# Optimization experiments

Measured on AMD Instinct MI355X. Metric: run time of the kernel, lower is better.

Reference implementation:

```python
import jax, jax.numpy as jnp
import numpy as np

N_TERMS = 500000
TERM_DIM = 300
N_RELS = 40
REL_DIM = 5
BATCH = 500000


def setup_inputs() -> dict:
    key = jax.random.key(0)
    k1, k2, k3, k4, k5, k6 = jax.random.split(key, 6)
    rels = jax.random.randint(k1, (BATCH,), 0, N_RELS)
    terms_L = jax.random.randint(k2, (BATCH,), 0, N_TERMS)
    terms_R = jax.random.randint(k3, (BATCH,), 0, N_TERMS)
    # learned parameters (nn.Embedding weights + assoc tensor)
    term_table = jax.random.normal(k4, (N_TERMS, TERM_DIM), dtype=jnp.float32) * 0.1
    rel_table = jax.random.normal(k5, (N_RELS, REL_DIM), dtype=jnp.float32) * 0.1
    assoc = jax.random.normal(k6, (REL_DIM, TERM_DIM, TERM_DIM), dtype=jnp.float32) * 0.01
    return {
        "rels": rels,
        "terms_L": terms_L,
        "terms_R": terms_R,
        "term_table": term_table,
        "rel_table": rel_table,
        "assoc": assoc,
    }


def reference(rels, terms_L, terms_R, term_table, rel_table, assoc):
    # Gather embeddings
    r = rel_table[rels]          # [B, 5]
    tL = term_table[terms_L]     # [B, D]
    tR = term_table[terms_R]     # [B, D]
    # Trilinear energy: energy_b = sum_{i,j,k} r[b,i] * assoc[i,j,k] * tL[b,j] * tR[b,k]
    # Contract through the small rank-5 relation axis to avoid the original's
    # [B, D, D] intermediate: tmp is only [B, 5, D].
    tmp = jnp.einsum('bj,rjk->brk', tL, assoc)   # [B, 5, D]
    energy = jnp.einsum('brk,bk,br->b', tmp, tR, r)  # [B]
    return energy
```

## Files before the change

### kernel.cpp

```cpp
#include <hip/hip_runtime.h>
#include <hip/hip_bf16.h>

#define DIMT 300
#define DPAD 320
#define NRELS 40
#define RELD 5
#define TILE_M 64
#define MAX_CHUNKS 8192

typedef __attribute__((ext_vector_type(8))) short bf16x8;
typedef __attribute__((ext_vector_type(4))) float f32x4;

#define DESC_OFF 256
#define SORTED_OFF (DESC_OFF + 3*MAX_CHUNKS)
#define MT_OFF_BYTES(B) ((((size_t)(SORTED_OFF + (B)) * 4) + 255) & ~(size_t)255)

__global__ void k_init(int* cnt) {
    int t = threadIdx.x;
    if (t < 64) cnt[t] = 0;
    if (t < 64) cnt[64 + t] = 0;
    if (t == 0) cnt[128] = 0;
}

__global__ void k_hist(const int* __restrict__ rels, int n, int* cnt) {
    __shared__ int l[NRELS];
    int t = threadIdx.x;
    if (t < NRELS) l[t] = 0;
    __syncthreads();
    int b = blockIdx.x * 256 + t;
    if (b < n) atomicAdd(&l[rels[b]], 1);
    __syncthreads();
    if (t < NRELS && l[t]) atomicAdd(&cnt[t], l[t]);
}

__global__ void k_scan(const int* __restrict__ cnt, int* cursor, int* n_chunks,
                       int* desc_rel, int* desc_start, int* desc_end) {
    __shared__ int offs[NRELS + 1];
    __shared__ int coff[NRELS + 1];
    if (threadIdx.x == 0) {
        int s = 0, c = 0;
        for (int r = 0; r < NRELS; r++) {
            offs[r] = s; s += cnt[r];
            coff[r] = c; c += (cnt[r] + TILE_M - 1) / TILE_M;
        }
        offs[NRELS] = s; coff[NRELS] = c;
        *n_chunks = c;
    }
    __syncthreads();
    if (threadIdx.x < NRELS) cursor[threadIdx.x] = offs[threadIdx.x];
    for (int r = 0; r < NRELS; r++) {
        int nch = (cnt[r] + TILE_M - 1) / TILE_M;
        int cend = offs[r] + cnt[r];
        for (int c = threadIdx.x; c < nch; c += 256) {
            int st = offs[r] + c * TILE_M;
            desc_rel[coff[r] + c] = r;
            desc_start[coff[r] + c] = st;
            desc_end[coff[r] + c] = min(st + TILE_M, cend);
        }
    }
}

__global__ void k_scatter(const int* __restrict__ rels, int n, int* cursor,
                          int* __restrict__ sorted) {
    __shared__ int l[NRELS];
    __shared__ int base[NRELS];
    int t = threadIdx.x;
    if (t < NRELS) l[t] = 0;
    __syncthreads();
    int b = blockIdx.x * 256 + t;
    int r = -1, loc = 0;
    if (b < n) { r = rels[b]; loc = atomicAdd(&l[r], 1); }
    __syncthreads();
    if (t < NRELS && l[t]) base[t] = atomicAdd(&cursor[t], l[t]);
    __syncthreads();
    if (b < n) sorted[base[r] + loc] = b;
}

__global__ void k_build_mt(const float* __restrict__ rel_table,
                           const float* __restrict__ assoc,
                           __hip_bfloat16* __restrict__ Mt) {
    int r = blockIdx.x / 100;
    int t6 = blockIdx.x % 100;
    int tn = (t6 / 10) * 32, tj = (t6 % 10) * 32;
    __shared__ float tile[32][33];
    __shared__ float rw[RELD];
    if (threadIdx.x < RELD) rw[threadIdx.x] = rel_table[r * RELD + threadIdx.x];
    __syncthreads();
    for (int e = threadIdx.x; e < 1024; e += 256) {
        int jl = e >> 5, nl = e & 31;
        int j = tj + jl, n = tn + nl;
        float v = 0.f;
        if (j < DIMT && n < DIMT) {
            #pragma unroll
            for (int i = 0; i < RELD; i++) v += rw[i] * assoc[(i * DIMT + j) * DIMT + n];
        }
        tile[jl][nl] = v;
    }
    __syncthreads();
    for (int e = threadIdx.x; e < 1024; e += 256) {
        int nl = e >> 5, jl = e & 31;
        int n = tn + nl, j = tj + jl;
        Mt[((size_t)r * DPAD + n) * DPAD + j] = __float2bfloat16(tile[jl][nl]);
    }
}

__device__ inline void async_g2l16(const void* g, void* l) {
    __builtin_amdgcn_global_load_lds(
        (const __attribute__((address_space(1))) unsigned int*)g,
        (__attribute__((address_space(3))) unsigned int*)l, 16, 0, 0);
}

__global__ __launch_bounds__(256, 3) void k_gemm(
    const int* __restrict__ sorted, const int* __restrict__ desc_rel,
    const int* __restrict__ desc_start, const int* __restrict__ desc_end,
    const int* __restrict__ n_chunks,
    const int* __restrict__ terms_L, const int* __restrict__ terms_R,
    const float* __restrict__ term_table, const __hip_bfloat16* __restrict__ Mt,
    float* __restrict__ out) {
    int cid = blockIdx.x;
    if (cid >= *n_chunks) return;
    int rel = desc_rel[cid];
    int start = desc_start[cid];
    int tm = desc_end[cid] - start;

    __shared__ __align__(16) __hip_bfloat16 Blds[2][DPAD * 32];
    __shared__ int elds[TILE_M];

    int t = threadIdx.x;
    if (t < TILE_M) elds[t] = (t < tm) ? sorted[start + t] : -1;
    __syncthreads();

    int wave = t >> 6, lane = t & 63;
    int quad = lane >> 4, l16 = lane & 15;

    const __hip_bfloat16* Mtr = Mt + (size_t)rel * DPAD * DPAD;

    auto stage = [&](int kc, int buf) {
        const char* gb = (const char*)Mtr + kc * 64;
        char* lb = (char*)&Blds[buf][0];
        #pragma unroll
        for (int i = 0; i < 5; i++) {
            int c = t + i * 256;
            async_g2l16(gb + (size_t)(c >> 2) * (DPAD * 2) + (c & 3) * 16,
                        lb + c * 16);
        }
    };

    stage(0, 0);

    int arow = wave * 16 + l16;
    int ae = elds[arow];
    const float* arp = (ae >= 0) ? (term_table + (size_t)terms_L[ae] * DIMT) : nullptr;
    bf16x8 afrag[10];
    #pragma unroll
    for (int kc = 0; kc < 10; kc++) {
        int kb = kc * 32 + quad * 8;
        float v[8];
        if (arp && kb + 8 <= DIMT) {
            float4 p0 = *(const float4*)(arp + kb);
            float4 p1 = *(const float4*)(arp + kb + 4);
            v[0] = p0.x; v[1] = p0.y; v[2] = p0.z; v[3] = p0.w;
            v[4] = p1.x; v[5] = p1.y; v[6] = p1.z; v[7] = p1.w;
        } else if (arp) {
            #pragma unroll
            for (int j = 0; j < 8; j++) v[j] = (kb + j < DIMT) ? arp[kb + j] : 0.f;
        } else {
            #pragma unroll
            for (int j = 0; j < 8; j++) v[j] = 0.f;
        }
        union { bf16x8 v8; __hip_bfloat16 h[8]; } u;
        #pragma unroll
        for (int j = 0; j < 8; j++) u.h[j] = __float2bfloat16(v[j]);
        afrag[kc] = u.v8;
    }

    f32x4 acc[20];
    #pragma unroll
    for (int i = 0; i < 20; i++) acc[i] = (f32x4){0.f, 0.f, 0.f, 0.f};

    __syncthreads();

    for (int kc = 0; kc < 10; kc++) {
        int cur = kc & 1;
        if (kc < 9) stage(kc + 1, cur ^ 1);
        const __hip_bfloat16* bb = &Blds[cur][0];
        #pragma unroll
        for (int nt = 0; nt < 20; nt++) {
            bf16x8 bfrag = *((const bf16x8*)(bb + (nt * 16 + l16) * 32 + quad * 8));
            acc[nt] = __builtin_amdgcn_mfma_f32_16x16x32_bf16(afrag[kc], bfrag, acc[nt], 0, 0, 0);
        }
        __syncthreads();
    }

    #pragma unroll
    for (int reg = 0; reg < 4; reg++) {
        int mrow = wave * 16 + quad * 4 + reg;
        int e = elds[mrow];
        float s = 0.f;
        if (e >= 0) {
            const float* tr = term_table + (size_t)terms_R[e] * DIMT;
            #pragma unroll
            for (int nt = 0; nt < 20; nt++) {
                int n = nt * 16 + l16;
                if (n < DIMT) s += acc[nt][reg] * tr[n];
            }
        }
        s += __shfl_xor(s, 1);
        s += __shfl_xor(s, 2);
        s += __shfl_xor(s, 4);
        s += __shfl_xor(s, 8);
        if (l16 == 0 && e >= 0) out[e] = s;
    }
}

extern "C" void kernel_launch(void* const* d_in, const int* in_sizes, int n_in,
                              void* d_out, int out_size, void* d_ws, size_t ws_size,
                              hipStream_t stream) {
    const int*   rels       = (const int*)d_in[0];
    const int*   terms_L    = (const int*)d_in[1];
    const int*   terms_R    = (const int*)d_in[2];
    const float* term_table = (const float*)d_in[3];
    const float* rel_table  = (const float*)d_in[4];
    const float* assoc      = (const float*)d_in[5];
    float* out = (float*)d_out;
    int B = in_sizes[0];

    int* wsi        = (int*)d_ws;
    int* cnt        = wsi;
    int* cursor     = wsi + 64;
    int* n_chunks   = wsi + 128;
    int* desc_rel   = wsi + DESC_OFF;
    int* desc_start = desc_rel + MAX_CHUNKS;
    int* desc_end   = desc_start + MAX_CHUNKS;
    int* sorted     = wsi + SORTED_OFF;
    __hip_bfloat16* Mt = (__hip_bfloat16*)((char*)d_ws + MT_OFF_BYTES(B));

    int nb = (B + 255) / 256;
    k_init<<<1, 128, 0, stream>>>(cnt);
    k_hist<<<nb, 256, 0, stream>>>(rels, B, cnt);
    k_scan<<<1, 256, 0, stream>>>(cnt, cursor, n_chunks, desc_rel, desc_start, desc_end);
    k_scatter<<<nb, 256, 0, stream>>>(rels, B, cursor, sorted);
    k_build_mt<<<NRELS * 100, 256, 0, stream>>>(rel_table, assoc, Mt);
    k_gemm<<<MAX_CHUNKS, 256, 0, stream>>>(sorted, desc_rel, desc_start, desc_end,
                                           n_chunks, terms_L, terms_R, term_table, Mt, out);
}
```

Before: 1.071 ms.

## Restructure GEMM loop over N panels with fused per-panel energy reduction and swizzled LDS

The GEMM kernel now runs 512-thread blocks over 128-row tiles, which halves the grid. It loops over 32-column panels of the relation matrix, each spanning the full K range, instead of over K chunks with 20 live accumulators. Each panel's product is immediately dotted with the gathered right-term embeddings into a running energy, which cuts accumulator register pressure and is meant to allow higher occupancy. The stored matrix is XOR-swizzled in 16-byte groups so the row-major LDS panel reads avoid bank conflicts. The tradeoff is that right-term gathers are issued inside the loop with scattered per-panel loads, and the first-panel staging is now double-issued up front.

```diff
diff --git a/kernel.cpp b/kernel.cpp
--- a/kernel.cpp
+++ b/kernel.cpp
@@ -5,8 +5,9 @@
 #define DPAD 320
 #define NRELS 40
 #define RELD 5
-#define TILE_M 64
+#define TILE_M 128
 #define MAX_CHUNKS 8192
+#define GEMM_GRID 4096
 
 typedef __attribute__((ext_vector_type(8))) short bf16x8;
 typedef __attribute__((ext_vector_type(4))) float f32x4;
@@ -100,7 +101,8 @@
     for (int e = threadIdx.x; e < 1024; e += 256) {
         int nl = e >> 5, jl = e & 31;
         int n = tn + nl, j = tj + jl;
-        Mt[((size_t)r * DPAD + n) * DPAD + j] = __float2bfloat16(tile[jl][nl]);
+        int sj = (((j >> 3) ^ (n & 7)) << 3) | (j & 7);
+        Mt[((size_t)r * DPAD + n) * DPAD + sj] = __float2bfloat16(tile[jl][nl]);
     }
 }
 
@@ -110,7 +112,7 @@
         (__attribute__((address_space(3))) unsigned int*)l, 16, 0, 0);
 }
 
-__global__ __launch_bounds__(256, 3) void k_gemm(
+__global__ __launch_bounds__(512, 6) void k_gemm(
     const int* __restrict__ sorted, const int* __restrict__ desc_rel,
     const int* __restrict__ desc_start, const int* __restrict__ desc_end,
     const int* __restrict__ n_chunks,
@@ -123,30 +125,30 @@
     int start = desc_start[cid];
     int tm = desc_end[cid] - start;
 
-    __shared__ __align__(16) __hip_bfloat16 Blds[2][DPAD * 32];
+    __shared__ __align__(16) __hip_bfloat16 Blds[2][32 * DPAD];
     __shared__ int elds[TILE_M];
 
     int t = threadIdx.x;
     if (t < TILE_M) elds[t] = (t < tm) ? sorted[start + t] : -1;
-    __syncthreads();
 
     int wave = t >> 6, lane = t & 63;
     int quad = lane >> 4, l16 = lane & 15;
 
     const __hip_bfloat16* Mtr = Mt + (size_t)rel * DPAD * DPAD;
 
-    auto stage = [&](int kc, int buf) {
-        const char* gb = (const char*)Mtr + kc * 64;
+    auto stage = [&](int np, int buf) {
+        const char* gb = (const char*)Mtr + (size_t)np * (32 * DPAD * 2);
         char* lb = (char*)&Blds[buf][0];
-        #pragma unroll
-        for (int i = 0; i < 5; i++) {
-            int c = t + i * 256;
-            async_g2l16(gb + (size_t)(c >> 2) * (DPAD * 2) + (c & 3) * 16,
-                        lb + c * 16);
-        }
+        async_g2l16(gb + t * 16, lb + t * 16);
+        async_g2l16(gb + (t + 512) * 16, lb + (t + 512) * 16);
+        if (t < 256)
+            async_g2l16(gb + (t + 1024) * 16, lb + (t + 1024) * 16);
     };
 
+    __syncthreads();
+
     stage(0, 0);
+    stage(1, 1);
 
     int arow = wave * 16 + l16;
     int ae = elds[arow];
@@ -174,42 +176,55 @@
         afrag[kc] = u.v8;
     }
 
-    f32x4 acc[20];
-    #pragma unroll
-    for (int i = 0; i < 20; i++) acc[i] = (f32x4){0.f, 0.f, 0.f, 0.f};
-
-    __syncthreads();
-
-    for (int kc = 0; kc < 10; kc++) {
-        int cur = kc & 1;
-        if (kc < 9) stage(kc + 1, cur ^ 1);
-        const __hip_bfloat16* bb = &Blds[cur][0];
-        #pragma unroll
-        for (int nt = 0; nt < 20; nt++) {
-            bf16x8 bfrag = *((const bf16x8*)(bb + (nt * 16 + l16) * 32 + quad * 8));
-            acc[nt] = __builtin_amdgcn_mfma_f32_16x16x32_bf16(afrag[kc], bfrag, acc[nt], 0, 0, 0);
-        }
-        __syncthreads();
-    }
-
+    int troff[4];
     #pragma unroll
     for (int reg = 0; reg < 4; reg++) {
-        int mrow = wave * 16 + quad * 4 + reg;
-        int e = elds[mrow];
-        float s = 0.f;
-        if (e >= 0) {
-            const float* tr = term_table + (size_t)terms_R[e] * DIMT;
-            #pragma unroll
-            for (int nt = 0; nt < 20; nt++) {
-                int n = nt * 16 + l16;
-                if (n < DIMT) s += acc[nt][reg] * tr[n];
+        int er = elds[wave * 16 + quad * 4 + reg];
+        troff[reg] = (er >= 0) ? (int)((size_t)terms_R[er] * DIMT) : -1;
+    }
+
+    float en[4] = {0.f, 0.f, 0.f, 0.f};
+
+    __syncthreads();
+
+    int sw = (l16 & 7) << 4;
+    for (int np = 0; np < 10; np++) {
+        int cur = np & 1;
+        if (np >= 1 && np <= 8) stage(np + 1, cur ^ 1);
+        const char* bb = (const char*)&Blds[cur][0];
+        f32x4 acc0 = {0.f, 0.f, 0.f, 0.f};
+        f32x4 acc1 = {0.f, 0.f, 0.f, 0.f};
+        #pragma unroll
+        for (int kc = 0; kc < 10; kc++) {
+            int jcb = (kc * 4 + quad) << 4;
+            bf16x8 b0 = *(const bf16x8*)(bb + l16 * (DPAD * 2) + (jcb ^ sw));
+            bf16x8 b1 = *(const bf16x8*)(bb + (16 + l16) * (DPAD * 2) + (jcb ^ sw));
+            acc0 = __builtin_amdgcn_mfma_f32_16x16x32_bf16(afrag[kc], b0, acc0, 0, 0, 0);
+            acc1 = __builtin_amdgcn_mfma_f32_16x16x32_bf16(afrag[kc], b1, acc1, 0, 0, 0);
+        }
+        int c0 = np * 32 + l16, c1 = c0 + 16;
+        #pragma unroll
+        for (int reg = 0; reg < 4; reg++) {
+            if (troff[reg] >= 0) {
+                float t0 = (c0 < DIMT) ? term_table[troff[reg] + c0] : 0.f;
+                float t1 = (c1 < DIMT) ? term_table[troff[reg] + c1] : 0.f;
+                en[reg] += acc0[reg] * t0 + acc1[reg] * t1;
             }
         }
+        __syncthreads();
+    }
+
+    #pragma unroll
+    for (int reg = 0; reg < 4; reg++) {
+        float s = en[reg];
         s += __shfl_xor(s, 1);
         s += __shfl_xor(s, 2);
         s += __shfl_xor(s, 4);
         s += __shfl_xor(s, 8);
-        if (l16 == 0 && e >= 0) out[e] = s;
+        if (l16 == 0) {
+            int e = elds[wave * 16 + quad * 4 + reg];
+            if (e >= 0) out[e] = s;
+        }
     }
 }
 
@@ -241,6 +256,6 @@
     k_scan<<<1, 256, 0, stream>>>(cnt, cursor, n_chunks, desc_rel, desc_start, desc_end);
     k_scatter<<<nb, 256, 0, stream>>>(rels, B, cursor, sorted);
     k_build_mt<<<NRELS * 100, 256, 0, stream>>>(rel_table, assoc, Mt);
-    k_gemm<<<MAX_CHUNKS, 256, 0, stream>>>(sorted, desc_rel, desc_start, desc_end,
-                                           n_chunks, terms_L, terms_R, term_table, Mt, out);
-}
+    k_gemm<<<GEMM_GRID, 512, 0, stream>>>(sorted, desc_rel, desc_start, desc_end,
+                                          n_chunks, terms_L, terms_R, term_table, Mt, out);
+}
```

Result: slower. 1.187 ms (+10.9%).

## Load GEMM B fragments directly from global memory instead of LDS staging

Applied to the files above, without the earlier changes.

Removes the double-buffered async global-to-LDS staging of the per-relation Mt matrix and the per-k-step barriers. Each wave now reads its bf16 B fragments straight from global memory (expected to hit L2 since Mt is small and shared across chunks of the same relation), and the row-index list is read from global memory instead of shared memory. This drops LDS traffic and synchronization but makes each wave fetch the full B tile independently, quadrupling global/L2 load traffic and exposing load latency without explicit prefetch.

```diff
diff --git a/kernel.cpp b/kernel.cpp
--- a/kernel.cpp
+++ b/kernel.cpp
@@ -102,12 +102,6 @@
         int n = tn + nl, j = tj + jl;
         Mt[((size_t)r * DPAD + n) * DPAD + j] = __float2bfloat16(tile[jl][nl]);
     }
-}
-
-__device__ inline void async_g2l16(const void* g, void* l) {
-    __builtin_amdgcn_global_load_lds(
-        (const __attribute__((address_space(1))) unsigned int*)g,
-        (__attribute__((address_space(3))) unsigned int*)l, 16, 0, 0);
 }
 
 __global__ __launch_bounds__(256, 3) void k_gemm(
@@ -123,33 +117,14 @@
     int start = desc_start[cid];
     int tm = desc_end[cid] - start;
 
-    __shared__ __align__(16) __hip_bfloat16 Blds[2][DPAD * 32];
-    __shared__ int elds[TILE_M];
-
-    int t = threadIdx.x;
-    if (t < TILE_M) elds[t] = (t < tm) ? sorted[start + t] : -1;
-    __syncthreads();
-
+    int t = threadIdx.x;
     int wave = t >> 6, lane = t & 63;
     int quad = lane >> 4, l16 = lane & 15;
 
     const __hip_bfloat16* Mtr = Mt + (size_t)rel * DPAD * DPAD;
 
-    auto stage = [&](int kc, int buf) {
-        const char* gb = (const char*)Mtr + kc * 64;
-        char* lb = (char*)&Blds[buf][0];
-        #pragma unroll
-        for (int i = 0; i < 5; i++) {
-            int c = t + i * 256;
-            async_g2l16(gb + (size_t)(c >> 2) * (DPAD * 2) + (c & 3) * 16,
-                        lb + c * 16);
-        }
-    };
-
-    stage(0, 0);
-
     int arow = wave * 16 + l16;
-    int ae = elds[arow];
+    int ae = (arow < tm) ? sorted[start + arow] : -1;
     const float* arp = (ae >= 0) ? (term_table + (size_t)terms_L[ae] * DIMT) : nullptr;
     bf16x8 afrag[10];
     #pragma unroll
@@ -178,24 +153,21 @@
     #pragma unroll
     for (int i = 0; i < 20; i++) acc[i] = (f32x4){0.f, 0.f, 0.f, 0.f};
 
-    __syncthreads();
-
+    const char* bl = (const char*)Mtr + (size_t)l16 * (DPAD * 2) + quad * 16;
+    #pragma unroll
     for (int kc = 0; kc < 10; kc++) {
-        int cur = kc & 1;
-        if (kc < 9) stage(kc + 1, cur ^ 1);
-        const __hip_bfloat16* bb = &Blds[cur][0];
+        const char* bk = bl + kc * 64;
         #pragma unroll
         for (int nt = 0; nt < 20; nt++) {
-            bf16x8 bfrag = *((const bf16x8*)(bb + (nt * 16 + l16) * 32 + quad * 8));
+            bf16x8 bfrag = *(const bf16x8*)(bk + (size_t)nt * (16 * DPAD * 2));
             acc[nt] = __builtin_amdgcn_mfma_f32_16x16x32_bf16(afrag[kc], bfrag, acc[nt], 0, 0, 0);
         }
-        __syncthreads();
     }
 
     #pragma unroll
     for (int reg = 0; reg < 4; reg++) {
         int mrow = wave * 16 + quad * 4 + reg;
-        int e = elds[mrow];
+        int e = (mrow < tm) ? sorted[start + mrow] : -1;
         float s = 0.f;
         if (e >= 0) {
             const float* tr = term_table + (size_t)terms_R[e] * DIMT;
```

After: 1.633 ms. 1.53x slower.
